# Kernel optimization log

Measured on AMD Instinct MI355X. Metric: run time of the kernel, lower is better.

Reference implementation:

```python
import jax, jax.numpy as jnp
import numpy as np
from jax import lax
import math

B, C, H, W, HEADS = 4, 64, 48, 48, 4
CH = C * HEADS
EPS_IN = 1e-5   # InstanceNorm2d eps
EPS_LN = 1e-5   # LayerNorm eps
EPS_NRM = 1e-12 # F.normalize eps


def setup_inputs() -> dict:
    key = jax.random.key(0)
    ks = jax.random.split(key, 8)
    rn = lambda k, shape, s: (jax.random.normal(k, shape, jnp.float32) * s)
    return {
        "emb_all": jax.random.normal(ks[0], (B, C, H, W), jnp.float32),
        "ln_w": jnp.ones((C,), jnp.float32),
        "ln_b": jnp.zeros((C,), jnp.float32),
        "wq": rn(ks[1], (CH, C), 0.05),
        "wk": rn(ks[2], (CH, C), 0.05),
        "wv": rn(ks[3], (CH, C), 0.05),
        "dwq": rn(ks[4], (CH, 1, 3, 3), 0.1),
        "dwk": rn(ks[5], (CH, 1, 3, 3), 0.1),
        "dwv": rn(ks[6], (CH, 1, 3, 3), 0.1),
        "proj_w": rn(ks[7], (C, C), 0.05),
        "proj_b": jnp.zeros((C,), jnp.float32),
    }


def _layernorm_c(x, w, b):
    # Restormer-style 'WithBias' LayerNorm over channel dim of NCHW
    mu = jnp.mean(x, axis=1, keepdims=True)
    var = jnp.mean((x - mu) ** 2, axis=1, keepdims=True)
    xn = (x - mu) / jnp.sqrt(var + EPS_LN)
    return xn * w[None, :, None, None] + b[None, :, None, None]


def _dwconv3(x, k):
    # depthwise 3x3, padding=1, NCHW / OIHW
    return lax.conv_general_dilated(
        x, k, window_strides=(1, 1), padding="SAME",
        feature_group_count=CH,
        dimension_numbers=("NCHW", "OIHW", "NCHW"))


def _qkv_branch(x, w1x1, dw):
    y = jnp.einsum("bchw,oc->bohw", x, w1x1)          # 1x1 conv, no bias
    y = _dwconv3(y, dw)                                # depthwise 3x3
    # b (head c) h w -> b head (h w) c
    y = y.reshape(B, HEADS, C, H * W).transpose(0, 1, 3, 2)
    return y


def reference(emb_all, ln_w, ln_b, wq, wk, wv, dwq, dwk, dwv, proj_w, proj_b):
    org = emb_all
    x = _layernorm_c(emb_all, ln_w, ln_b)

    q = _qkv_branch(x, wq, dwq)   # (B, HEADS, HW, C)
    k = _qkv_branch(x, wk, dwk)
    v = _qkv_branch(x, wv, dwv)

    # L2-normalize along channel dim (F.normalize semantics)
    q = q / jnp.maximum(jnp.linalg.norm(q, axis=-1, keepdims=True), EPS_NRM)
    k = k / jnp.maximum(jnp.linalg.norm(k, axis=-1, keepdims=True), EPS_NRM)

    num = H * W
    atten = jnp.einsum("bhnc,bhmc->bhnm", q, k) / math.sqrt(num)

    # InstanceNorm2d over the (hw x hw) score map, per (batch, head), no affine
    mu = jnp.mean(atten, axis=(-2, -1), keepdims=True)
    var = jnp.mean((atten - mu) ** 2, axis=(-2, -1), keepdims=True)
    atten = (atten - mu) / jnp.sqrt(var + EPS_IN)

    probs = jax.nn.softmax(atten, axis=-1)

    out = jnp.einsum("bhnm,bhmc->bhnc", probs, v)      # (B, HEADS, HW, C)
    out = out.mean(axis=1)                             # average over heads
    out = out.transpose(0, 2, 1).reshape(B, C, H, W)   # b (h w) c -> b c h w
    out = jnp.einsum("bchw,oc->bohw", out, proj_w) + proj_b[None, :, None, None]
    return org + out
```

## Files before the change

### kernel.cpp

```cpp
#include <hip/hip_runtime.h>
#include <hip/hip_bf16.h>
#include <math.h>

#define NB 4
#define NC 64
#define NH 48
#define NW 48
#define NHEADS 4
#define NCH 256
#define NHW 2304
#define NBH 16
#define NCHK 4
#define CHUNK 576
#define NT (CHUNK / 32)

#define OB_Y    0ull
#define OB_GP   0ull
#define OB_SQP  4718592ull
#define OB_OHP  0ull
#define OB_Q    18874368ull
#define OB_K    23592960ull
#define OB_V    28311552ull
#define OB_L    33030144ull
#define OB_SC   33619968ull

typedef __bf16 bf16x8 __attribute__((ext_vector_type(8)));
typedef float f32x4 __attribute__((ext_vector_type(4)));
typedef float f32x16 __attribute__((ext_vector_type(16)));

__device__ __forceinline__ float bf2f(ushort u) {
  return __uint_as_float(((unsigned)u) << 16);
}
__device__ __forceinline__ ushort f2bf(float f) {
  __hip_bfloat16 h = __float2bfloat16(f);
  return *(ushort*)&h;
}
__device__ __forceinline__ void gload16(const void* g, void* l) {
  __builtin_amdgcn_global_load_lds((const __attribute__((address_space(1))) unsigned int*)g,
                                   (__attribute__((address_space(3))) unsigned int*)l, 16, 0, 0);
}

__global__ __launch_bounds__(256) void k_lnconv(const float* __restrict__ emb,
                                                const float* __restrict__ lw,
                                                const float* __restrict__ lb,
                                                const float* __restrict__ wq,
                                                const float* __restrict__ wk,
                                                const float* __restrict__ wv,
                                                ushort* __restrict__ Y) {
  __shared__ float Xs[64][68];
  __shared__ float mu_s[64], rs_s[64], lw_s[64], lb_s[64];
  int p0 = blockIdx.x * 64, b = blockIdx.y, qkv = blockIdx.z;
  const float* Wm = qkv == 0 ? wq : (qkv == 1 ? wk : wv);
  const float* src = emb + (size_t)b * NC * NHW + p0;
  int t = threadIdx.x;
  for (int e = t; e < 1024; e += 256) {
    int c = e >> 4, p4 = (e & 15) * 4;
    float4 v = *(const float4*)&src[c * NHW + p4];
    Xs[p4][c] = v.x; Xs[p4 + 1][c] = v.y; Xs[p4 + 2][c] = v.z; Xs[p4 + 3][c] = v.w;
  }
  if (t < 64) { lw_s[t] = lw[t]; lb_s[t] = lb[t]; }
  __syncthreads();
  if (t < 64) {
    float s = 0.f, ss = 0.f;
#pragma unroll
    for (int c = 0; c < 64; c += 4) {
      float4 v = *(const float4*)&Xs[t][c];
      s += (v.x + v.y) + (v.z + v.w);
      ss += (v.x * v.x + v.y * v.y) + (v.z * v.z + v.w * v.w);
    }
    float m = s * (1.f / 64.f), va = ss * (1.f / 64.f) - m * m;
    mu_s[t] = m;
    rs_s[t] = rsqrtf(va + 1e-5f);
  }
  __syncthreads();
  int lane = t & 63, wvi = t >> 6, ql = lane & 31, h = lane >> 5;
  bf16x8 bfr[2][4];
#pragma unroll
  for (int pb = 0; pb < 2; ++pb) {
    int px = pb * 32 + ql;
    float mu = mu_s[px], rs = rs_s[px];
#pragma unroll
    for (int kc = 0; kc < 4; ++kc) {
      union { bf16x8 v; ushort u[8]; } pk;
#pragma unroll
      for (int j = 0; j < 8; ++j) {
        int c = kc * 16 + h * 8 + j;
        pk.u[j] = f2bf((Xs[px][c] - mu) * rs * lw_s[c] + lb_s[c]);
      }
      bfr[pb][kc] = pk.v;
    }
  }
  bf16x8 afr[2][4];
#pragma unroll
  for (int ob = 0; ob < 2; ++ob) {
    const float* wr = Wm + (size_t)(wvi * 64 + ob * 32 + ql) * 64;
#pragma unroll
    for (int kc = 0; kc < 4; ++kc) {
      union { bf16x8 v; ushort u[8]; } pk;
#pragma unroll
      for (int j = 0; j < 8; ++j) pk.u[j] = f2bf(wr[kc * 16 + h * 8 + j]);
      afr[ob][kc] = pk.v;
    }
  }
  f32x16 d00 = {}, d01 = {}, d10 = {}, d11 = {};
#pragma unroll
  for (int kc = 0; kc < 4; ++kc) {
    d00 = __builtin_amdgcn_mfma_f32_32x32x16_bf16(afr[0][kc], bfr[0][kc], d00, 0, 0, 0);
    d01 = __builtin_amdgcn_mfma_f32_32x32x16_bf16(afr[0][kc], bfr[1][kc], d01, 0, 0, 0);
    d10 = __builtin_amdgcn_mfma_f32_32x32x16_bf16(afr[1][kc], bfr[0][kc], d10, 0, 0, 0);
    d11 = __builtin_amdgcn_mfma_f32_32x32x16_bf16(afr[1][kc], bfr[1][kc], d11, 0, 0, 0);
  }
  ushort* dst = Y + ((size_t)(qkv * NB + b) * NCH + wvi * 64) * NHW + p0;
#pragma unroll
  for (int r = 0; r < 16; ++r) {
    int row = (r & 3) + 8 * (r >> 2) + 4 * h;
    dst[(size_t)row * NHW + ql] = f2bf(d00[r]);
    dst[(size_t)row * NHW + 32 + ql] = f2bf(d01[r]);
    dst[(size_t)(32 + row) * NHW + ql] = f2bf(d10[r]);
    dst[(size_t)(32 + row) * NHW + 32 + ql] = f2bf(d11[r]);
  }
}

__global__ __launch_bounds__(256) void k_dw(const ushort* __restrict__ Y,
                                            const float* __restrict__ dwq,
                                            const float* __restrict__ dwk,
                                            const float* __restrict__ dwv,
                                            ushort* __restrict__ Qo,
                                            ushort* __restrict__ Ko,
                                            ushort* __restrict__ Vo) {
  __shared__ ushort Ys[64][3][48];
  __shared__ float Zs[64][49];
  __shared__ float Rs[48];
  int h = blockIdx.x;
  int hd = blockIdx.y & 3, qkv = blockIdx.y >> 2;
  int b = blockIdx.z;
  int bh = b * NHEADS + hd;
  const float* dwp = qkv == 0 ? dwq : (qkv == 1 ? dwk : dwv);
  const ushort* src = Y + ((size_t)(qkv * NB + b) * NCH + hd * 64) * NHW;
  for (int e = threadIdx.x; e < 64 * 3 * 12; e += 256) {
    int c = e / 36, rem = e % 36, r = rem / 12, w4 = (rem % 12) * 4;
    int hh = h + r - 1;
    ushort4 v = (hh >= 0 && hh < NH) ? *(const ushort4*)&src[c * NHW + hh * NW + w4]
                                     : make_ushort4(0, 0, 0, 0);
    *(ushort4*)&Ys[c][r][w4] = v;
  }
  __syncthreads();
  for (int e = threadIdx.x; e < 64 * 48; e += 256) {
    int c = e / 48, w = e % 48;
    const float* kk = dwp + ((size_t)hd * 64 + c) * 9;
    float acc = 0.f;
#pragma unroll
    for (int r = 0; r < 3; ++r)
#pragma unroll
      for (int dx = 0; dx < 3; ++dx) {
        int ww = w + dx - 1;
        float yv = (ww >= 0 && ww < NW) ? bf2f(Ys[c][r][ww]) : 0.f;
        acc += yv * kk[r * 3 + dx];
      }
    Zs[c][w] = acc;
  }
  __syncthreads();
  if (qkv < 2) {
    if (threadIdx.x < 48) {
      int w = threadIdx.x;
      float ss = 0.f;
#pragma unroll
      for (int c = 0; c < 64; ++c) { float z = Zs[c][w]; ss += z * z; }
      Rs[w] = 1.f / fmaxf(sqrtf(ss), 1e-12f);
    }
    __syncthreads();
    ushort* dst = (qkv == 0 ? Qo : Ko) + (size_t)bh * NHW * 64;
    for (int e = threadIdx.x; e < 48 * 16; e += 256) {
      int w = e >> 4, c4 = (e & 15) * 4;
      float rsc = Rs[w];
      ushort4 u = make_ushort4(f2bf(Zs[c4][w] * rsc), f2bf(Zs[c4 + 1][w] * rsc),
                               f2bf(Zs[c4 + 2][w] * rsc), f2bf(Zs[c4 + 3][w] * rsc));
      *(ushort4*)&dst[((size_t)(c4 >> 3) * NHW + h * NW + w) * 8 + (c4 & 7)] = u;
    }
  } else {
    ushort* dst = Vo + (size_t)bh * NHW * 64;
    for (int e = threadIdx.x; e < 64 * 12; e += 256) {
      int c = e / 12, w4 = (e % 12) * 4;
      ushort4 u = make_ushort4(f2bf(Zs[c][w4]), f2bf(Zs[c][w4 + 1]),
                               f2bf(Zs[c][w4 + 2]), f2bf(Zs[c][w4 + 3]));
      *(ushort4*)&dst[((size_t)(h * 6 + (w4 >> 3)) * 64 + c) * 8 + (w4 & 7)] = u;
    }
  }
}

__global__ __launch_bounds__(256) void k_gram(const ushort* __restrict__ Q,
                                              const ushort* __restrict__ K,
                                              float* __restrict__ Gp,
                                              float* __restrict__ SQp) {
  __shared__ ushort Xt[64][72];
  int ns = blockIdx.x, qk = blockIdx.y, bh = blockIdx.z;
  const ushort* src = (qk ? K : Q) + (size_t)bh * NHW * 64;
  int t = threadIdx.x, lane = t & 63, wv = t >> 6;
  int lr = lane & 15, lg = lane >> 4;
  int ci0 = (wv >> 1) * 32, cj0 = (wv & 1) * 32;
  f32x4 acc[2][2];
#pragma unroll
  for (int i = 0; i < 2; ++i)
#pragma unroll
    for (int j = 0; j < 2; ++j) acc[i][j] = (f32x4){0.f, 0.f, 0.f, 0.f};
  float sq = 0.f;
  for (int it = 0; it < 4; ++it) {
    __syncthreads();
#pragma unroll
    for (int i2 = 0; i2 < 2; ++i2) {
      int n = t & 63, cg = (t >> 6) + 4 * i2;
      union { bf16x8 v; ushort u[8]; } ld;
      ld.v = *(const bf16x8*)&src[((size_t)cg * NHW + ns * 256 + it * 64 + n) * 8];
#pragma unroll
      for (int j = 0; j < 8; ++j) Xt[cg * 8 + j][n] = ld.u[j];
    }
    __syncthreads();
    if (t < 64) {
#pragma unroll
      for (int g = 0; g < 8; ++g) {
        union { bf16x8 v; ushort u[8]; } rd;
        rd.v = *(const bf16x8*)&Xt[t][g * 8];
#pragma unroll
        for (int j = 0; j < 8; ++j) sq += bf2f(rd.u[j]);
      }
    }
#pragma unroll
    for (int kh = 0; kh < 2; ++kh) {
      bf16x8 a0 = *(const bf16x8*)&Xt[ci0 + lr][kh * 32 + lg * 8];
      bf16x8 a1 = *(const bf16x8*)&Xt[ci0 + 16 + lr][kh * 32 + lg * 8];
      bf16x8 b0 = *(const bf16x8*)&Xt[cj0 + lr][kh * 32 + lg * 8];
      bf16x8 b1 = *(const bf16x8*)&Xt[cj0 + 16 + lr][kh * 32 + lg * 8];
      acc[0][0] = __builtin_amdgcn_mfma_f32_16x16x32_bf16(a0, b0, acc[0][0], 0, 0, 0);
      acc[0][1] = __builtin_amdgcn_mfma_f32_16x16x32_bf16(a0, b1, acc[0][1], 0, 0, 0);
      acc[1][0] = __builtin_amdgcn_mfma_f32_16x16x32_bf16(a1, b0, acc[1][0], 0, 0, 0);
      acc[1][1] = __builtin_amdgcn_mfma_f32_16x16x32_bf16(a1, b1, acc[1][1], 0, 0, 0);
    }
  }
  float* g = Gp + ((size_t)(ns * 2 + qk) * NBH + bh) * 4096;
#pragma unroll
  for (int ii = 0; ii < 2; ++ii)
#pragma unroll
    for (int jj = 0; jj < 2; ++jj)
#pragma unroll
      for (int r = 0; r < 4; ++r)
        g[(ci0 + ii * 16 + lg * 4 + r) * 64 + cj0 + jj * 16 + lr] = acc[ii][jj][r];
  if (t < 64) SQp[((size_t)(ns * 2 + qk) * NBH + bh) * 64 + t] = sq;
}

__global__ __launch_bounds__(256) void k_scale(const float* __restrict__ Gp,
                                               const float* __restrict__ SQp,
                                               float* __restrict__ SC) {
  __shared__ float red[256];
  __shared__ float red2[64];
  int bh = blockIdx.x, t = threadIdx.x;
  float ssum = 0.f;
  for (int i = t; i < 4096; i += 256) {
    float gq = 0.f, gk = 0.f;
#pragma unroll
    for (int ns = 0; ns < 9; ++ns) {
      gq += Gp[((size_t)(ns * 2 + 0) * NBH + bh) * 4096 + i];
      gk += Gp[((size_t)(ns * 2 + 1) * NBH + bh) * 4096 + i];
    }
    ssum += gq * gk;
  }
  red[t] = ssum;
  if (t < 64) {
    float sq_q = 0.f, sq_k = 0.f;
#pragma unroll
    for (int ns = 0; ns < 9; ++ns) {
      sq_q += SQp[((size_t)(ns * 2 + 0) * NBH + bh) * 64 + t];
      sq_k += SQp[((size_t)(ns * 2 + 1) * NBH + bh) * 64 + t];
    }
    red2[t] = sq_q * sq_k;
  }
  __syncthreads();
  if (t == 0) {
    double S = 0.0, A = 0.0;
    for (int i = 0; i < 256; ++i) S += red[i];
    for (int i = 0; i < 64; ++i) A += red2[i];
    const double N2 = (double)NHW * (double)NHW;
    double mean = A / (N2 * 48.0);
    double ea2 = S / (N2 * 2304.0);
    double var = ea2 - mean * mean;
    SC[bh] = (float)((1.0 / sqrt(var + 1e-5)) / 48.0 * 1.4426950408889634);
  }
}

__global__ __launch_bounds__(256, 2) void k_attn(const ushort* __restrict__ Q,
                                                 const ushort* __restrict__ K,
                                                 const ushort* __restrict__ V,
                                                 const float* __restrict__ SC,
                                                 ushort* __restrict__ OHp,
                                                 float* __restrict__ Lp) {
  __shared__ ushort Kl[4][2048];
  __shared__ ushort Vl[4][2048];
  int p = blockIdx.x;
  int gb = p & 7;
  int w = p >> 3;
  int qt = w % 18;
  int rem = w / 18;
  int chunk = rem & 3;
  int bh = gb * 2 + (rem >> 2);
  int t = threadIdx.x, lane = t & 63, wv = t >> 6;
  int ql = lane & 31, h = lane >> 5;
  int q0 = qt * 128 + wv * 32;
  int m00 = chunk * CHUNK;
  const ushort* base = Q + (size_t)bh * NHW * 64;
  float sc2 = SC[bh];

  bf16x8 qfr[4];
#pragma unroll
  for (int kc = 0; kc < 4; ++kc)
    qfr[kc] = *(const bf16x8*)&base[((size_t)(kc * 2 + h) * NHW + q0 + ql) * 8];
  asm volatile("s_waitcnt vmcnt(0)" ::: "memory");

  const ushort* kst = K + (size_t)bh * NHW * 64 + ((size_t)(wv * 2 + h) * NHW + m00 + ql) * 8;
  const ushort* vst = V + (size_t)bh * NHW * 64 + ((size_t)((m00 >> 3) + wv) * 64 + lane) * 8;

  f32x16 o0 = {}, o1 = {};
  float lp = 0.f;

  auto COMPUTE = [&](int cb) {
    bf16x8 ka[4], vb[4];
#pragma unroll
    for (int i = 0; i < 4; ++i)
      ka[i] = *(const bf16x8*)&Kl[cb][(2 * i + h) * 256 + ql * 8];
    vb[0] = *(const bf16x8*)&Vl[cb][h * 512 + ql * 8];
    vb[1] = *(const bf16x8*)&Vl[cb][(2 + h) * 512 + ql * 8];
    vb[2] = *(const bf16x8*)&Vl[cb][h * 512 + (ql + 32) * 8];
    vb[3] = *(const bf16x8*)&Vl[cb][(2 + h) * 512 + (ql + 32) * 8];
    __builtin_amdgcn_s_setprio(1);
    f32x16 s = {};
    s = __builtin_amdgcn_mfma_f32_32x32x16_bf16(ka[0], qfr[0], s, 0, 0, 0);
    s = __builtin_amdgcn_mfma_f32_32x32x16_bf16(ka[1], qfr[1], s, 0, 0, 0);
    s = __builtin_amdgcn_mfma_f32_32x32x16_bf16(ka[2], qfr[2], s, 0, 0, 0);
    s = __builtin_amdgcn_mfma_f32_32x32x16_bf16(ka[3], qfr[3], s, 0, 0, 0);
    __builtin_amdgcn_s_setprio(0);
    float pv[16];
    float l0 = 0.f, l1 = 0.f, l2 = 0.f, l3 = 0.f;
#pragma unroll
    for (int r = 0; r < 16; r += 4) {
      pv[r] = __builtin_exp2f(s[r] * sc2);
      pv[r + 1] = __builtin_exp2f(s[r + 1] * sc2);
      pv[r + 2] = __builtin_exp2f(s[r + 2] * sc2);
      pv[r + 3] = __builtin_exp2f(s[r + 3] * sc2);
      l0 += pv[r]; l1 += pv[r + 1]; l2 += pv[r + 2]; l3 += pv[r + 3];
    }
    lp += (l0 + l1) + (l2 + l3);
    uint u[8];
#pragma unroll
    for (int i = 0; i < 8; ++i)
      asm("v_cvt_pk_bf16_f32 %0, %1, %2" : "=v"(u[i]) : "v"(pv[2 * i]), "v"(pv[2 * i + 1]));
    asm volatile("v_permlane32_swap_b32 %0, %1" : "+v"(u[0]), "+v"(u[2]));
    asm volatile("v_permlane32_swap_b32 %0, %1" : "+v"(u[1]), "+v"(u[3]));
    asm volatile("v_permlane32_swap_b32 %0, %1" : "+v"(u[4]), "+v"(u[6]));
    asm volatile("v_permlane32_swap_b32 %0, %1" : "+v"(u[5]), "+v"(u[7]));
    union { uint uu[4]; bf16x8 v; } pa0, pa1;
    pa0.uu[0] = u[0]; pa0.uu[1] = u[1]; pa0.uu[2] = u[2]; pa0.uu[3] = u[3];
    pa1.uu[0] = u[4]; pa1.uu[1] = u[5]; pa1.uu[2] = u[6]; pa1.uu[3] = u[7];
    __builtin_amdgcn_s_setprio(1);
    o0 = __builtin_amdgcn_mfma_f32_32x32x16_bf16(pa0.v, vb[0], o0, 0, 0, 0);
    o0 = __builtin_amdgcn_mfma_f32_32x32x16_bf16(pa1.v, vb[1], o0, 0, 0, 0);
    o1 = __builtin_amdgcn_mfma_f32_32x32x16_bf16(pa0.v, vb[2], o1, 0, 0, 0);
    o1 = __builtin_amdgcn_mfma_f32_32x32x16_bf16(pa1.v, vb[3], o1, 0, 0, 0);
    __builtin_amdgcn_s_setprio(0);
  };

  gload16(kst, (void*)&Kl[0][wv * 512]);
  gload16(vst, (void*)&Vl[0][wv * 512]);
  gload16(kst + 256, (void*)&Kl[1][wv * 512]);
  gload16(vst + 2048, (void*)&Vl[1][wv * 512]);

  for (int mt = 0; mt < NT - 2; ++mt) {
    int sb = (mt + 2) & 3;
    gload16(kst + (size_t)(mt + 2) * 256, (void*)&Kl[sb][wv * 512]);
    gload16(vst + (size_t)(mt + 2) * 2048, (void*)&Vl[sb][wv * 512]);
    asm volatile("s_waitcnt vmcnt(4)" ::: "memory");
    __builtin_amdgcn_s_barrier();
    COMPUTE(mt & 3);
  }
  asm volatile("s_waitcnt vmcnt(2)" ::: "memory");
  __builtin_amdgcn_s_barrier();
  COMPUTE((NT - 2) & 3);
  asm volatile("s_waitcnt vmcnt(0)" ::: "memory");
  __builtin_amdgcn_s_barrier();
  COMPUTE((NT - 1) & 3);

  lp += __shfl_xor(lp, 32);
  if (h == 0) Lp[(size_t)(chunk * NBH + bh) * NHW + q0 + ql] = lp;
  ushort* od = OHp + ((size_t)(chunk * NBH + bh) * NHW + q0) * 64;
#pragma unroll
  for (int r = 0; r < 16; ++r) {
    int qrow = (r & 3) + 8 * (r >> 2) + 4 * h;
    od[(size_t)qrow * 64 + ql] = f2bf(o0[r]);
    od[(size_t)qrow * 64 + 32 + ql] = f2bf(o1[r]);
  }
}

__global__ __launch_bounds__(256) void k_proj(const ushort* __restrict__ OHp,
                                              const float* __restrict__ Lp,
                                              const float* __restrict__ PW,
                                              const float* __restrict__ PB,
                                              const float* __restrict__ org,
                                              float* __restrict__ out) {
  __shared__ float Ls[4][4][16];
  __shared__ float linv[4][16];
  __shared__ float Ms[64][17];
  int p0 = blockIdx.x * 16, b = blockIdx.y;
  int t = threadIdx.x;
  {
    int ck = t >> 6, hd = (t >> 4) & 3, p = t & 15;
    Ls[ck][hd][p] = Lp[(size_t)(ck * NBH + b * 4 + hd) * NHW + p0 + p];
  }
  __syncthreads();
  if (t < 64) {
    int hd = t >> 4, p = t & 15;
    linv[hd][p] = 1.f / (Ls[0][hd][p] + Ls[1][hd][p] + Ls[2][hd][p] + Ls[3][hd][p]);
  }
  __syncthreads();
  {
    int p = t >> 4, c4 = (t & 15) * 4;
    float a0 = 0.f, a1 = 0.f, a2 = 0.f, a3 = 0.f;
#pragma unroll
    for (int hd = 0; hd < 4; ++hd) {
      float s0 = 0.f, s1 = 0.f, s2 = 0.f, s3 = 0.f;
#pragma unroll
      for (int ck = 0; ck < 4; ++ck) {
        ushort4 u = *(const ushort4*)&OHp[((size_t)(ck * NBH + b * 4 + hd) * NHW + p0 + p) * 64 + c4];
        s0 += bf2f(u.x); s1 += bf2f(u.y); s2 += bf2f(u.z); s3 += bf2f(u.w);
      }
      float li = linv[hd][p];
      a0 += s0 * li; a1 += s1 * li; a2 += s2 * li; a3 += s3 * li;
    }
    Ms[c4][p] = 0.25f * a0;
    Ms[c4 + 1][p] = 0.25f * a1;
    Ms[c4 + 2][p] = 0.25f * a2;
    Ms[c4 + 3][p] = 0.25f * a3;
  }
  __syncthreads();
  int p = t & 15, og = t >> 4;
  float acc[4];
#pragma unroll
  for (int i = 0; i < 4; ++i) acc[i] = PB[og * 4 + i];
  for (int c = 0; c < 64; ++c) {
    float xr = Ms[c][p];
#pragma unroll
    for (int i = 0; i < 4; ++i) acc[i] += PW[(og * 4 + i) * 64 + c] * xr;
  }
  const float* orgp = org + (size_t)b * NC * NHW + p0 + p;
  float* outp = out + (size_t)b * NC * NHW + p0 + p;
#pragma unroll
  for (int i = 0; i < 4; ++i) {
    int oc = og * 4 + i;
    outp[(size_t)oc * NHW] = orgp[(size_t)oc * NHW] + acc[i];
  }
}

extern "C" void kernel_launch(void* const* d_in, const int* in_sizes, int n_in,
                              void* d_out, int out_size, void* d_ws, size_t ws_size,
                              hipStream_t stream) {
  const float* emb = (const float*)d_in[0];
  const float* lnw = (const float*)d_in[1];
  const float* lnb = (const float*)d_in[2];
  const float* wq  = (const float*)d_in[3];
  const float* wk  = (const float*)d_in[4];
  const float* wv  = (const float*)d_in[5];
  const float* dwq = (const float*)d_in[6];
  const float* dwk = (const float*)d_in[7];
  const float* dwv = (const float*)d_in[8];
  const float* pw  = (const float*)d_in[9];
  const float* pb  = (const float*)d_in[10];
  char* ws = (char*)d_ws;
  ushort* Y   = (ushort*)(ws + OB_Y);
  float*  Gp  = (float*)(ws + OB_GP);
  float*  SQp = (float*)(ws + OB_SQP);
  ushort* OHp = (ushort*)(ws + OB_OHP);
  ushort* Qb  = (ushort*)(ws + OB_Q);
  ushort* Kb  = (ushort*)(ws + OB_K);
  ushort* Vb  = (ushort*)(ws + OB_V);
  float*  Lpt = (float*)(ws + OB_L);
  float*  SCp = (float*)(ws + OB_SC);
  float* out = (float*)d_out;

  k_lnconv<<<dim3(NHW / 64, NB, 3), 256, 0, stream>>>(emb, lnw, lnb, wq, wk, wv, Y);
  k_dw<<<dim3(NH, 12, NB), 256, 0, stream>>>(Y, dwq, dwk, dwv, Qb, Kb, Vb);
  k_gram<<<dim3(9, 2, NBH), 256, 0, stream>>>(Qb, Kb, Gp, SQp);
  k_scale<<<dim3(NBH), 256, 0, stream>>>(Gp, SQp, SCp);
  k_attn<<<dim3(1152), 256, 0, stream>>>(Qb, Kb, Vb, SCp, OHp, Lpt);
  k_proj<<<dim3(NHW / 16, NB), 256, 0, stream>>>(OHp, Lpt, pw, pb, emb, out);
}
```

Measured before the change: 114.9 us.

## Vectorize depthwise conv, atomic-reduce Gram partials, and double-step attention pipeline

The depthwise conv now stages the 3x3 weights in shared memory and computes four outputs per thread from packed bf16 loads. The per-position norm reduction is split across four channel groups. The Gram kernel accumulates into one zeroed buffer with atomicAdd, which adds a memset and shrinks the scale kernel to a simple reduction with wavefront shuffles. The attention loop now processes two K/V tiles per barrier, with full vmcnt waits and two split row-sum accumulators. This trades finer-grained load overlap for fewer barriers.

```diff
diff --git a/kernel.cpp b/kernel.cpp
--- a/kernel.cpp
+++ b/kernel.cpp
@@ -15,8 +15,8 @@
 #define NT (CHUNK / 32)
 
 #define OB_Y    0ull
-#define OB_GP   0ull
-#define OB_SQP  4718592ull
+#define OB_G    0ull
+#define OB_SQ   524288ull
 #define OB_OHP  0ull
 #define OB_Q    18874368ull
 #define OB_K    23592960ull
@@ -129,7 +129,9 @@
                                             ushort* __restrict__ Ko,
                                             ushort* __restrict__ Vo) {
   __shared__ ushort Ys[64][3][48];
-  __shared__ float Zs[64][49];
+  __shared__ float Zs[64][50];
+  __shared__ float Ks9[64][9];
+  __shared__ float Rp[4][48];
   __shared__ float Rs[48];
   int h = blockIdx.x;
   int hd = blockIdx.y & 3, qkv = blockIdx.y >> 2;
@@ -137,7 +139,9 @@
   int bh = b * NHEADS + hd;
   const float* dwp = qkv == 0 ? dwq : (qkv == 1 ? dwk : dwv);
   const ushort* src = Y + ((size_t)(qkv * NB + b) * NCH + hd * 64) * NHW;
-  for (int e = threadIdx.x; e < 64 * 3 * 12; e += 256) {
+  int t = threadIdx.x;
+  for (int e = t; e < 576; e += 256) Ks9[e / 9][e % 9] = dwp[(size_t)hd * 576 + e];
+  for (int e = t; e < 2304; e += 256) {
     int c = e / 36, rem = e % 36, r = rem / 12, w4 = (rem % 12) * 4;
     int hh = h + r - 1;
     ushort4 v = (hh >= 0 && hh < NH) ? *(const ushort4*)&src[c * NHW + hh * NW + w4]
@@ -145,32 +149,47 @@
     *(ushort4*)&Ys[c][r][w4] = v;
   }
   __syncthreads();
-  for (int e = threadIdx.x; e < 64 * 48; e += 256) {
-    int c = e / 48, w = e % 48;
-    const float* kk = dwp + ((size_t)hd * 64 + c) * 9;
-    float acc = 0.f;
-#pragma unroll
-    for (int r = 0; r < 3; ++r)
-#pragma unroll
-      for (int dx = 0; dx < 3; ++dx) {
-        int ww = w + dx - 1;
-        float yv = (ww >= 0 && ww < NW) ? bf2f(Ys[c][r][ww]) : 0.f;
-        acc += yv * kk[r * 3 + dx];
-      }
-    Zs[c][w] = acc;
+  for (int e = t; e < 768; e += 256) {
+    int c = e / 12, w4 = (e % 12) * 4;
+    float acc0 = 0.f, acc1 = 0.f, acc2 = 0.f, acc3 = 0.f;
+#pragma unroll
+    for (int r = 0; r < 3; ++r) {
+      const ushort* row = &Ys[c][r][0];
+      int li = w4 >= 4 ? w4 - 4 : 0;
+      int ri = w4 <= 40 ? w4 + 4 : 40;
+      uint2 L = *(const uint2*)&row[li];
+      uint2 M = *(const uint2*)&row[w4];
+      uint2 R = *(const uint2*)&row[ri];
+      float vm1 = (w4 == 0) ? 0.f : __uint_as_float(L.y & 0xffff0000u);
+      float m0 = __uint_as_float(M.x << 16);
+      float m1 = __uint_as_float(M.x & 0xffff0000u);
+      float m2 = __uint_as_float(M.y << 16);
+      float m3 = __uint_as_float(M.y & 0xffff0000u);
+      float v4 = (w4 == 44) ? 0.f : __uint_as_float(R.x << 16);
+      float k0 = Ks9[c][r * 3], k1 = Ks9[c][r * 3 + 1], k2 = Ks9[c][r * 3 + 2];
+      acc0 += vm1 * k0 + m0 * k1 + m1 * k2;
+      acc1 += m0 * k0 + m1 * k1 + m2 * k2;
+      acc2 += m1 * k0 + m2 * k1 + m3 * k2;
+      acc3 += m2 * k0 + m3 * k1 + v4 * k2;
+    }
+    *(float2*)&Zs[c][w4] = make_float2(acc0, acc1);
+    *(float2*)&Zs[c][w4 + 2] = make_float2(acc2, acc3);
   }
   __syncthreads();
   if (qkv < 2) {
-    if (threadIdx.x < 48) {
-      int w = threadIdx.x;
+    if (t < 192) {
+      int cq = t / 48, w = t % 48;
       float ss = 0.f;
 #pragma unroll
-      for (int c = 0; c < 64; ++c) { float z = Zs[c][w]; ss += z * z; }
-      Rs[w] = 1.f / fmaxf(sqrtf(ss), 1e-12f);
-    }
+      for (int i = 0; i < 16; ++i) { float z = Zs[cq * 16 + i][w]; ss += z * z; }
+      Rp[cq][w] = ss;
+    }
+    __syncthreads();
+    if (t < 48)
+      Rs[t] = 1.f / fmaxf(sqrtf(Rp[0][t] + Rp[1][t] + Rp[2][t] + Rp[3][t]), 1e-12f);
     __syncthreads();
     ushort* dst = (qkv == 0 ? Qo : Ko) + (size_t)bh * NHW * 64;
-    for (int e = threadIdx.x; e < 48 * 16; e += 256) {
+    for (int e = t; e < 768; e += 256) {
       int w = e >> 4, c4 = (e & 15) * 4;
       float rsc = Rs[w];
       ushort4 u = make_ushort4(f2bf(Zs[c4][w] * rsc), f2bf(Zs[c4 + 1][w] * rsc),
@@ -179,10 +198,10 @@
     }
   } else {
     ushort* dst = Vo + (size_t)bh * NHW * 64;
-    for (int e = threadIdx.x; e < 64 * 12; e += 256) {
+    for (int e = t; e < 768; e += 256) {
       int c = e / 12, w4 = (e % 12) * 4;
-      ushort4 u = make_ushort4(f2bf(Zs[c][w4]), f2bf(Zs[c][w4 + 1]),
-                               f2bf(Zs[c][w4 + 2]), f2bf(Zs[c][w4 + 3]));
+      float4 z = *(const float4*)&Zs[c][w4];
+      ushort4 u = make_ushort4(f2bf(z.x), f2bf(z.y), f2bf(z.z), f2bf(z.w));
       *(ushort4*)&dst[((size_t)(h * 6 + (w4 >> 3)) * 64 + c) * 8 + (w4 & 7)] = u;
     }
   }
@@ -190,8 +209,8 @@
 
 __global__ __launch_bounds__(256) void k_gram(const ushort* __restrict__ Q,
                                               const ushort* __restrict__ K,
-                                              float* __restrict__ Gp,
-                                              float* __restrict__ SQp) {
+                                              float* __restrict__ G,
+                                              float* __restrict__ SQ) {
   __shared__ ushort Xt[64][72];
   int ns = blockIdx.x, qk = blockIdx.y, bh = blockIdx.z;
   const ushort* src = (qk ? K : Q) + (size_t)bh * NHW * 64;
@@ -236,53 +255,41 @@
       acc[1][1] = __builtin_amdgcn_mfma_f32_16x16x32_bf16(a1, b1, acc[1][1], 0, 0, 0);
     }
   }
-  float* g = Gp + ((size_t)(ns * 2 + qk) * NBH + bh) * 4096;
+  float* g = G + ((size_t)qk * NBH + bh) * 4096;
 #pragma unroll
   for (int ii = 0; ii < 2; ++ii)
 #pragma unroll
     for (int jj = 0; jj < 2; ++jj)
 #pragma unroll
       for (int r = 0; r < 4; ++r)
-        g[(ci0 + ii * 16 + lg * 4 + r) * 64 + cj0 + jj * 16 + lr] = acc[ii][jj][r];
-  if (t < 64) SQp[((size_t)(ns * 2 + qk) * NBH + bh) * 64 + t] = sq;
-}
-
-__global__ __launch_bounds__(256) void k_scale(const float* __restrict__ Gp,
-                                               const float* __restrict__ SQp,
+        atomicAdd(&g[(ci0 + ii * 16 + lg * 4 + r) * 64 + cj0 + jj * 16 + lr], acc[ii][jj][r]);
+  if (t < 64) atomicAdd(&SQ[((size_t)qk * NBH + bh) * 64 + t], sq);
+}
+
+__global__ __launch_bounds__(256) void k_scale(const float* __restrict__ G,
+                                               const float* __restrict__ SQ,
                                                float* __restrict__ SC) {
   __shared__ float red[256];
-  __shared__ float red2[64];
   int bh = blockIdx.x, t = threadIdx.x;
   float ssum = 0.f;
-  for (int i = t; i < 4096; i += 256) {
-    float gq = 0.f, gk = 0.f;
-#pragma unroll
-    for (int ns = 0; ns < 9; ++ns) {
-      gq += Gp[((size_t)(ns * 2 + 0) * NBH + bh) * 4096 + i];
-      gk += Gp[((size_t)(ns * 2 + 1) * NBH + bh) * 4096 + i];
-    }
-    ssum += gq * gk;
-  }
+  for (int i = t; i < 4096; i += 256)
+    ssum += G[(size_t)bh * 4096 + i] * G[(size_t)(NBH + bh) * 4096 + i];
   red[t] = ssum;
+  __syncthreads();
+  if (t < 128) red[t] += red[t + 128];
+  __syncthreads();
   if (t < 64) {
-    float sq_q = 0.f, sq_k = 0.f;
-#pragma unroll
-    for (int ns = 0; ns < 9; ++ns) {
-      sq_q += SQp[((size_t)(ns * 2 + 0) * NBH + bh) * 64 + t];
-      sq_k += SQp[((size_t)(ns * 2 + 1) * NBH + bh) * 64 + t];
-    }
-    red2[t] = sq_q * sq_k;
-  }
-  __syncthreads();
-  if (t == 0) {
-    double S = 0.0, A = 0.0;
-    for (int i = 0; i < 256; ++i) S += red[i];
-    for (int i = 0; i < 64; ++i) A += red2[i];
-    const double N2 = (double)NHW * (double)NHW;
-    double mean = A / (N2 * 48.0);
-    double ea2 = S / (N2 * 2304.0);
-    double var = ea2 - mean * mean;
-    SC[bh] = (float)((1.0 / sqrt(var + 1e-5)) / 48.0 * 1.4426950408889634);
+    float v = red[t] + red[t + 64];
+    float v2 = SQ[bh * 64 + t] * SQ[(NBH + bh) * 64 + t];
+#pragma unroll
+    for (int m = 32; m; m >>= 1) { v += __shfl_xor(v, m); v2 += __shfl_xor(v2, m); }
+    if (t == 0) {
+      const double N2 = (double)NHW * (double)NHW;
+      double mean = (double)v2 / (N2 * 48.0);
+      double ea2 = (double)v / (N2 * 2304.0);
+      double var = ea2 - mean * mean;
+      SC[bh] = (float)((1.0 / sqrt(var + 1e-5)) / 48.0 * 1.4426950408889634);
+    }
   }
 }
 
@@ -318,9 +325,13 @@
   const ushort* vst = V + (size_t)bh * NHW * 64 + ((size_t)((m00 >> 3) + wv) * 64 + lane) * 8;
 
   f32x16 o0 = {}, o1 = {};
-  float lp = 0.f;
-
-  auto COMPUTE = [&](int cb) {
+  float lpA = 0.f, lpB = 0.f;
+
+  auto STAGE = [&](int tt) {
+    gload16(kst + (size_t)tt * 256, (void*)&Kl[tt & 3][wv * 512]);
+    gload16(vst + (size_t)tt * 2048, (void*)&Vl[tt & 3][wv * 512]);
+  };
+  auto COMPUTE = [&](int cb, float& lpr) {
     bf16x8 ka[4], vb[4];
 #pragma unroll
     for (int i = 0; i < 4; ++i)
@@ -346,7 +357,7 @@
       pv[r + 3] = __builtin_exp2f(s[r + 3] * sc2);
       l0 += pv[r]; l1 += pv[r + 1]; l2 += pv[r + 2]; l3 += pv[r + 3];
     }
-    lp += (l0 + l1) + (l2 + l3);
+    lpr += (l0 + l1) + (l2 + l3);
     uint u[8];
 #pragma unroll
     for (int i = 0; i < 8; ++i)
@@ -366,26 +377,16 @@
     __builtin_amdgcn_s_setprio(0);
   };
 
-  gload16(kst, (void*)&Kl[0][wv * 512]);
-  gload16(vst, (void*)&Vl[0][wv * 512]);
-  gload16(kst + 256, (void*)&Kl[1][wv * 512]);
-  gload16(vst + 2048, (void*)&Vl[1][wv * 512]);
-
-  for (int mt = 0; mt < NT - 2; ++mt) {
-    int sb = (mt + 2) & 3;
-    gload16(kst + (size_t)(mt + 2) * 256, (void*)&Kl[sb][wv * 512]);
-    gload16(vst + (size_t)(mt + 2) * 2048, (void*)&Vl[sb][wv * 512]);
-    asm volatile("s_waitcnt vmcnt(4)" ::: "memory");
+  STAGE(0); STAGE(1);
+  for (int mt = 0; mt < NT; mt += 2) {
+    asm volatile("s_waitcnt vmcnt(0)" ::: "memory");
     __builtin_amdgcn_s_barrier();
-    COMPUTE(mt & 3);
-  }
-  asm volatile("s_waitcnt vmcnt(2)" ::: "memory");
-  __builtin_amdgcn_s_barrier();
-  COMPUTE((NT - 2) & 3);
-  asm volatile("s_waitcnt vmcnt(0)" ::: "memory");
-  __builtin_amdgcn_s_barrier();
-  COMPUTE((NT - 1) & 3);
-
+    if (mt + 2 < NT) { STAGE(mt + 2); STAGE(mt + 3); }
+    COMPUTE(mt & 3, lpA);
+    COMPUTE((mt + 1) & 3, lpB);
+  }
+
+  float lp = lpA + lpB;
   lp += __shfl_xor(lp, 32);
   if (h == 0) Lp[(size_t)(chunk * NBH + bh) * NHW + q0 + ql] = lp;
   ushort* od = OHp + ((size_t)(chunk * NBH + bh) * NHW + q0) * 64;
@@ -472,8 +473,8 @@
   const float* pb  = (const float*)d_in[10];
   char* ws = (char*)d_ws;
   ushort* Y   = (ushort*)(ws + OB_Y);
-  float*  Gp  = (float*)(ws + OB_GP);
-  float*  SQp = (float*)(ws + OB_SQP);
+  float*  G   = (float*)(ws + OB_G);
+  float*  SQ  = (float*)(ws + OB_SQ);
   ushort* OHp = (ushort*)(ws + OB_OHP);
   ushort* Qb  = (ushort*)(ws + OB_Q);
   ushort* Kb  = (ushort*)(ws + OB_K);
@@ -484,8 +485,9 @@
 
   k_lnconv<<<dim3(NHW / 64, NB, 3), 256, 0, stream>>>(emb, lnw, lnb, wq, wk, wv, Y);
   k_dw<<<dim3(NH, 12, NB), 256, 0, stream>>>(Y, dwq, dwk, dwv, Qb, Kb, Vb);
-  k_gram<<<dim3(9, 2, NBH), 256, 0, stream>>>(Qb, Kb, Gp, SQp);
-  k_scale<<<dim3(NBH), 256, 0, stream>>>(Gp, SQp, SCp);
+  hipMemsetAsync(G, 0, 532480, stream);
+  k_gram<<<dim3(9, 2, NBH), 256, 0, stream>>>(Qb, Kb, G, SQ);
+  k_scale<<<dim3(NBH), 256, 0, stream>>>(G, SQ, SCp);
   k_attn<<<dim3(1152), 256, 0, stream>>>(Qb, Kb, Vb, SCp, OHp, Lpt);
   k_proj<<<dim3(NHW / 16, NB), 256, 0, stream>>>(OHp, Lpt, pw, pb, emb, out);
 }
```

New measurement: 108.7 us. -5.4%, faster.
